# Optimization experiments

Measured on AMD Instinct MI355X. Metric: run time of the kernel, lower is better.

Reference implementation:

```python
import jax, jax.numpy as jnp
import numpy as np

N = 50000   # nodes
E = 800000  # edges
B = 512     # graphs
EPS = 1e-5  # BatchNorm eps


def _p(k, shape, scale=0.05):
    return jax.random.normal(k, shape, dtype=jnp.float32) * scale


def setup_inputs() -> dict:
    key = jax.random.key(0)
    ks = jax.random.split(key, 24)
    inp = {
        "x": jax.random.normal(ks[0], (N, 4), dtype=jnp.float32),
        "edge_index": jax.random.randint(ks[1], (2, E), 0, N, dtype=jnp.int64),
        "edge_weight": jax.random.uniform(ks[2], (E,), dtype=jnp.float32),
        "batch": jnp.sort(jax.random.randint(ks[3], (N,), 0, B, dtype=jnp.int64)),
        # block1: GCNConv(4,64) + BN + shortcut Linear(4,64)
        "W1": _p(ks[4], (4, 64)), "b1": jnp.zeros((64,), jnp.float32),
        "g1": jnp.ones((64,), jnp.float32), "be1": jnp.zeros((64,), jnp.float32),
        "sW1": _p(ks[5], (4, 64)), "sb1": jnp.zeros((64,), jnp.float32),
        # block2: GCNConv(64,64) + BN, identity shortcut
        "W2": _p(ks[6], (64, 64)), "b2": jnp.zeros((64,), jnp.float32),
        "g2": jnp.ones((64,), jnp.float32), "be2": jnp.zeros((64,), jnp.float32),
        # block3: GCNConv(64,128) + BN + shortcut Linear(64,128)
        "W3": _p(ks[7], (64, 128)), "b3": jnp.zeros((128,), jnp.float32),
        "g3": jnp.ones((128,), jnp.float32), "be3": jnp.zeros((128,), jnp.float32),
        "sW3": _p(ks[8], (64, 128)), "sb3": jnp.zeros((128,), jnp.float32),
        # head: Linear(256,128) + BN + ReLU + Linear(128,1)
        "fW1": _p(ks[9], (256, 128)), "fb1": jnp.zeros((128,), jnp.float32),
        "fg": jnp.ones((128,), jnp.float32), "fbe": jnp.zeros((128,), jnp.float32),
        "fW2": _p(ks[10], (128, 1)), "fb2": jnp.zeros((1,), jnp.float32),
    }
    return inp


def _bn(x, g, b):
    # training-mode BatchNorm1d over node dim (biased variance)
    m = x.mean(0)
    v = x.var(0)
    return (x - m) * jax.lax.rsqrt(v + EPS) * g + b


def _gcn(x, W, b, src, dst, w, n):
    # PyG GCNConv: add self-loops (weight 1), symmetric normalization
    h = x @ W  # [n, out]
    loop = jnp.arange(n)
    s = jnp.concatenate([src, loop])
    d = jnp.concatenate([dst, loop])
    ww = jnp.concatenate([w, jnp.ones((n,), x.dtype)])
    deg = jax.ops.segment_sum(ww, d, num_segments=n)
    dis = jnp.where(deg > 0, jax.lax.rsqrt(jnp.maximum(deg, EPS)), 0.0)
    norm = dis[s] * ww * dis[d]  # [E+n]
    return jax.ops.segment_sum(h[s] * norm[:, None], d, num_segments=n) + b


def _block(x, W, b, g, be, sW, sb, src, dst, w, n):
    out = jax.nn.relu(_bn(_gcn(x, W, b, src, dst, w, n), g, be))
    sc = x if sW is None else x @ sW + sb
    return out + sc


def reference(x, edge_index, edge_weight, batch,
              W1, b1, g1, be1, sW1, sb1,
              W2, b2, g2, be2,
              W3, b3, g3, be3, sW3, sb3,
              fW1, fb1, fg, fbe, fW2, fb2):
    n = x.shape[0]
    src, dst = edge_index[0], edge_index[1]
    h = _block(x, W1, b1, g1, be1, sW1, sb1, src, dst, edge_weight, n)
    h = _block(h, W2, b2, g2, be2, None, None, src, dst, edge_weight, n)
    h = _block(h, W3, b3, g3, be3, sW3, sb3, src, dst, edge_weight, n)
    # global mean / max pooling per graph
    cnt = jax.ops.segment_sum(jnp.ones((n,), h.dtype), batch, num_segments=B)
    p1 = jax.ops.segment_sum(h, batch, num_segments=B) / jnp.maximum(cnt, 1.0)[:, None]
    p2 = jax.ops.segment_max(h, batch, num_segments=B)
    z = jnp.concatenate([p1, p2], axis=1)  # [B, 256]
    z = jax.nn.relu(_bn(z @ fW1 + fb1, fg, fbe))  # Dropout eval = identity
    return z @ fW2 + fb2  # [B, 1]
```

## Files before the change

### kernel.cpp

```cpp
#include <hip/hip_runtime.h>

#define BNEPS 1e-5f


__global__ void k_fill(float* p, int n, float v){
  int i = blockIdx.x*blockDim.x + threadIdx.x;
  if(i < n) p[i] = v;
}


__global__ void k_count(int* cnt, const int* __restrict__ dst, int E){
  int e = blockIdx.x*blockDim.x + threadIdx.x;
  if(e < E) atomicAdd(&cnt[dst[e]], 1);
}

__global__ void k_scan1(int* cnt, int* rowptr, int* bsum, int n){
  __shared__ int sh[256];
  int tid = threadIdx.x;
  int i = blockIdx.x*256 + tid;
  int v = (i < n) ? cnt[i] : 0;
  sh[tid] = v;
  __syncthreads();
  for(int o = 1; o < 256; o <<= 1){
    int t = (tid >= o) ? sh[tid-o] : 0;
    __syncthreads();
    sh[tid] += t;
    __syncthreads();
  }
  if(i < n){ rowptr[i] = sh[tid] - v; cnt[i] = 0; }
  if(tid == 255) bsum[blockIdx.x] = sh[255];
}

__global__ void k_scan2(int* bsum, int m){
  __shared__ int sh[256];
  int tid = threadIdx.x;
  int v = (tid < m) ? bsum[tid] : 0;
  sh[tid] = v;
  __syncthreads();
  for(int o = 1; o < 256; o <<= 1){
    int t = (tid >= o) ? sh[tid-o] : 0;
    __syncthreads();
    sh[tid] += t;
    __syncthreads();
  }
  if(tid < m) bsum[tid] = sh[tid] - v;
}

__global__ void k_scan3(int* rowptr, const int* bsum, int n, int E){
  int i = blockIdx.x*blockDim.x + threadIdx.x;
  if(i < n) rowptr[i] += bsum[i >> 8];
  if(i == 0) rowptr[n] = E;
}

__global__ void k_scatter2(const int* __restrict__ src, const int* __restrict__ dst,
                           const float* __restrict__ w, const int* __restrict__ rowptr,
                           int* cur, int2* __restrict__ erec, int E){
  int e = blockIdx.x*blockDim.x + threadIdx.x;
  if(e >= E) return;
  int d = dst[e];
  int idx = rowptr[d] + atomicAdd(&cur[d], 1);
  erec[idx] = make_int2(src[e], __float_as_int(w[e]));
}

__global__ void k_degdis(const int2* __restrict__ erec, const int* __restrict__ rowptr,
                         float* __restrict__ dis, int n){
  int i = blockIdx.x*blockDim.x + threadIdx.x;
  if(i >= n) return;
  float s = 1.0f;
  int e0 = rowptr[i], e1 = rowptr[i+1];
  for(int j = e0; j < e1; j++) s += __int_as_float(erec[j].y);
  dis[i] = rsqrtf(s);
}

__global__ void k_mknorm(int2* __restrict__ erec, const int* __restrict__ rowptr,
                         const float* __restrict__ dis, int n){
  int i = blockIdx.x*blockDim.x + threadIdx.x;
  if(i >= n) return;
  float di = dis[i];
  int e0 = rowptr[i], e1 = rowptr[i+1];
  for(int j = e0; j < e1; j++){
    int2 r = erec[j];
    erec[j].y = __float_as_int(dis[r.x] * __int_as_float(r.y) * di);
  }
}


__global__ __launch_bounds__(256)
void k_gcn1_fused(const float* __restrict__ X, const float* __restrict__ dis,
                  const int* __restrict__ rowptr, const int2* __restrict__ erec,
                  const float* __restrict__ W, const float* __restrict__ bias,
                  float* __restrict__ H, float* __restrict__ stats, int n){
  const int tid = threadIdx.x;
  const int lane = tid & 63;
  const int wid = tid >> 6;
  const int eg = lane >> 2;
  const int ch = lane & 3;
  const float w0 = W[lane], w1 = W[64+lane], w2 = W[128+lane], w3 = W[192+lane];
  const float bc = bias[lane];
  float s = 0.f, s2 = 0.f;
  for(int i = blockIdx.x*4 + wid; i < n; i += gridDim.x*4){
    int e0 = rowptr[i], e1 = rowptr[i+1];
    float acc = 0.f;
    for(int j = e0 + eg; j < e1; j += 16){
      int2 r = erec[j];
      acc += X[(size_t)r.x*4 + ch] * __int_as_float(r.y);
    }
    if(eg == 0){
      float d = dis[i];
      acc += X[(size_t)i*4 + ch] * d * d;
    }
    acc += __shfl_xor(acc, 4);
    acc += __shfl_xor(acc, 8);
    acc += __shfl_xor(acc, 16);
    acc += __shfl_xor(acc, 32);
    float p0 = __shfl(acc, 0), p1 = __shfl(acc, 1);
    float p2 = __shfl(acc, 2), p3 = __shfl(acc, 3);
    float h = bc + p0*w0 + p1*w1 + p2*w2 + p3*w3;
    H[(size_t)i*64 + lane] = h;
    s += h; s2 += h*h;
  }
  __shared__ float rs[256], rs2[256];
  rs[tid] = s; rs2[tid] = s2;
  __syncthreads();
  if(tid < 64){
    atomicAdd(&stats[tid],    rs[tid]+rs[tid+64]+rs[tid+128]+rs[tid+192]);
    atomicAdd(&stats[64+tid], rs2[tid]+rs2[tid+64]+rs2[tid+128]+rs2[tid+192]);
  }
}


template<int C>
__global__ void k_gather(const float* __restrict__ H, const float* __restrict__ dis,
                         const int* __restrict__ rowptr, const int2* __restrict__ erec,
                         float* __restrict__ P, int n){
  const int NPB = 256 / C;
  int i = blockIdx.x*NPB + threadIdx.x / C;
  int c = threadIdx.x % C;
  if(i >= n) return;
  float di = dis[i];
  float acc = H[(size_t)i*C + c]*di*di;
  int e0 = rowptr[i], e1 = rowptr[i+1];
  int j = e0;
  for(; j + 8 <= e1; j += 8){
    int2 r0 = erec[j],   r1 = erec[j+1], r2 = erec[j+2], r3 = erec[j+3];
    int2 r4 = erec[j+4], r5 = erec[j+5], r6 = erec[j+6], r7 = erec[j+7];
    float h0 = H[(size_t)r0.x*C + c];
    float h1 = H[(size_t)r1.x*C + c];
    float h2 = H[(size_t)r2.x*C + c];
    float h3 = H[(size_t)r3.x*C + c];
    float h4 = H[(size_t)r4.x*C + c];
    float h5 = H[(size_t)r5.x*C + c];
    float h6 = H[(size_t)r6.x*C + c];
    float h7 = H[(size_t)r7.x*C + c];
    acc += h0*__int_as_float(r0.y) + h1*__int_as_float(r1.y)
         + h2*__int_as_float(r2.y) + h3*__int_as_float(r3.y)
         + h4*__int_as_float(r4.y) + h5*__int_as_float(r5.y)
         + h6*__int_as_float(r6.y) + h7*__int_as_float(r7.y);
  }
  for(; j < e1; j++){
    int2 r = erec[j];
    acc += H[(size_t)r.x*C + c] * __int_as_float(r.y);
  }
  P[(size_t)i*C + c] = acc;
}


template<int C>
__global__ __launch_bounds__(256)
void k_gemm_tile(const float* __restrict__ X, const float* __restrict__ W,
                 const float* __restrict__ bias, float* __restrict__ H,
                 float* __restrict__ stats, int n, int ntiles){
  const int RR = C/16;
  const int CG = C/4;
  __shared__ float Xs[64*65];
  __shared__ float Ws[64*C];
  __shared__ float sst[2*C];
  const int tid = threadIdx.x;
  const int cg = tid % CG, rg = tid / CG;
  const int c0 = cg*4;
  for(int t = tid; t < 16*C; t += 256)
    reinterpret_cast<float4*>(Ws)[t] = reinterpret_cast<const float4*>(W)[t];
  const float4 bc = *reinterpret_cast<const float4*>(bias + c0);
  float sacc[4] = {0,0,0,0}, qacc[4] = {0,0,0,0};
  const float4* X4 = reinterpret_cast<const float4*>(X);
  for(int tile = blockIdx.x; tile < ntiles; tile += gridDim.x){
    const int r0 = tile*64;
    __syncthreads();
    #pragma unroll
    for(int q = 0; q < 4; q++){
      int idx = tid + q*256;
      int row = idx >> 4, k4 = idx & 15;
      float4 v = (r0+row < n) ? X4[(size_t)(r0+row)*16 + k4] : make_float4(0.f,0.f,0.f,0.f);
      Xs[(4*k4+0)*65 + row] = v.x;
      Xs[(4*k4+1)*65 + row] = v.y;
      Xs[(4*k4+2)*65 + row] = v.z;
      Xs[(4*k4+3)*65 + row] = v.w;
    }
    __syncthreads();
    float acc[RR][4];
    #pragma unroll
    for(int r = 0; r < RR; r++){ acc[r][0]=bc.x; acc[r][1]=bc.y; acc[r][2]=bc.z; acc[r][3]=bc.w; }
    #pragma unroll 8
    for(int k = 0; k < 64; k++){
      float4 wv = reinterpret_cast<const float4*>(Ws)[k*CG + cg];
      #pragma unroll
      for(int r = 0; r < RR; r++){
        float xv = Xs[k*65 + rg*RR + r];
        acc[r][0] = fmaf(xv, wv.x, acc[r][0]);
        acc[r][1] = fmaf(xv, wv.y, acc[r][1]);
        acc[r][2] = fmaf(xv, wv.z, acc[r][2]);
        acc[r][3] = fmaf(xv, wv.w, acc[r][3]);
      }
    }
    #pragma unroll
    for(int r = 0; r < RR; r++){
      int row = r0 + rg*RR + r;
      if(row < n){
        *reinterpret_cast<float4*>(H + (size_t)row*C + c0) =
            make_float4(acc[r][0], acc[r][1], acc[r][2], acc[r][3]);
        #pragma unroll
        for(int j = 0; j < 4; j++){ sacc[j] += acc[r][j]; qacc[j] += acc[r][j]*acc[r][j]; }
      }
    }
  }
  for(int t = tid; t < 2*C; t += 256) sst[t] = 0.f;
  __syncthreads();
  #pragma unroll
  for(int j = 0; j < 4; j++){
    atomicAdd(&sst[c0+j], sacc[j]);
    atomicAdd(&sst[C+c0+j], qacc[j]);
  }
  __syncthreads();
  for(int t = tid; t < 2*C; t += 256) atomicAdd(&stats[t], sst[t]);
}

template<int C>
__global__ __launch_bounds__(256)
void k_gemm_bnsc_tile(const float* __restrict__ X, const float* __restrict__ sW,
                      const float* __restrict__ sb,
                      const float* __restrict__ agg, const float* __restrict__ stats,
                      const float* __restrict__ g, const float* __restrict__ be,
                      float* __restrict__ out, int n, int ntiles){
  const int RR = C/16;
  const int CG = C/4;
  __shared__ float Xs[64*65];
  __shared__ float Ws[64*C];
  const int tid = threadIdx.x;
  const int cg = tid % CG, rg = tid / CG;
  const int c0 = cg*4;
  for(int t = tid; t < 16*C; t += 256)
    reinterpret_cast<float4*>(Ws)[t] = reinterpret_cast<const float4*>(sW)[t];
  const float4 bc = *reinterpret_cast<const float4*>(sb + c0);
  float scal[4], shft[4];
  {
    float invn = 1.0f / n;
    #pragma unroll
    for(int j = 0; j < 4; j++){
      float m = stats[c0+j]*invn;
      float v = stats[C+c0+j]*invn - m*m;
      float rs = rsqrtf(v + BNEPS) * g[c0+j];
      scal[j] = rs;
      shft[j] = be[c0+j] - m*rs;
    }
  }
  const float4* X4 = reinterpret_cast<const float4*>(X);
  for(int tile = blockIdx.x; tile < ntiles; tile += gridDim.x){
    const int r0 = tile*64;
    __syncthreads();
    #pragma unroll
    for(int q = 0; q < 4; q++){
      int idx = tid + q*256;
      int row = idx >> 4, k4 = idx & 15;
      float4 v = (r0+row < n) ? X4[(size_t)(r0+row)*16 + k4] : make_float4(0.f,0.f,0.f,0.f);
      Xs[(4*k4+0)*65 + row] = v.x;
      Xs[(4*k4+1)*65 + row] = v.y;
      Xs[(4*k4+2)*65 + row] = v.z;
      Xs[(4*k4+3)*65 + row] = v.w;
    }
    __syncthreads();
    float acc[RR][4];
    #pragma unroll
    for(int r = 0; r < RR; r++){ acc[r][0]=bc.x; acc[r][1]=bc.y; acc[r][2]=bc.z; acc[r][3]=bc.w; }
    #pragma unroll 8
    for(int k = 0; k < 64; k++){
      float4 wv = reinterpret_cast<const float4*>(Ws)[k*CG + cg];
      #pragma unroll
      for(int r = 0; r < RR; r++){
        float xv = Xs[k*65 + rg*RR + r];
        acc[r][0] = fmaf(xv, wv.x, acc[r][0]);
        acc[r][1] = fmaf(xv, wv.y, acc[r][1]);
        acc[r][2] = fmaf(xv, wv.z, acc[r][2]);
        acc[r][3] = fmaf(xv, wv.w, acc[r][3]);
      }
    }
    #pragma unroll
    for(int r = 0; r < RR; r++){
      int row = r0 + rg*RR + r;
      if(row < n){
        float4 a = *reinterpret_cast<const float4*>(agg + (size_t)row*C + c0);
        float4 o;
        o.x = fmaxf(a.x*scal[0] + shft[0], 0.f) + acc[r][0];
        o.y = fmaxf(a.y*scal[1] + shft[1], 0.f) + acc[r][1];
        o.z = fmaxf(a.z*scal[2] + shft[2], 0.f) + acc[r][2];
        o.w = fmaxf(a.w*scal[3] + shft[3], 0.f) + acc[r][3];
        *reinterpret_cast<float4*>(out + (size_t)row*C + c0) = o;
      }
    }
  }
}


template<int C>
__global__ void k_bn_add4(const float* __restrict__ agg, const float* __restrict__ stats,
                          const float* __restrict__ g, const float* __restrict__ be,
                          const float* __restrict__ add, float* __restrict__ out, int n){
  int idx = blockIdx.x*blockDim.x + threadIdx.x;
  if(idx >= n*(C/4)) return;
  int c = (idx % (C/4))*4;
  float invn = 1.0f / n;
  float4 sm = *reinterpret_cast<const float4*>(stats + c);
  float4 sq = *reinterpret_cast<const float4*>(stats + C + c);
  float4 g4 = *reinterpret_cast<const float4*>(g + c);
  float4 b4 = *reinterpret_cast<const float4*>(be + c);
  float4 a  = reinterpret_cast<const float4*>(agg)[idx];
  float4 ad = reinterpret_cast<const float4*>(add)[idx];
  float4 o;
  #define BN1(X) { float m = sm.X*invn; float v = sq.X*invn - m*m; \
    o.X = fmaxf((a.X-m)*rsqrtf(v+BNEPS)*g4.X + b4.X, 0.f) + ad.X; }
  BN1(x) BN1(y) BN1(z) BN1(w)
  #undef BN1
  reinterpret_cast<float4*>(out)[idx] = o;
}

__global__ void k_bn_sc4_v4(const float* __restrict__ agg, const float* __restrict__ stats,
                            const float* __restrict__ g, const float* __restrict__ be,
                            const float* __restrict__ X, const float* __restrict__ sW,
                            const float* __restrict__ sb, float* __restrict__ out, int n){
  int idx = blockIdx.x*blockDim.x + threadIdx.x;
  if(idx >= n*16) return;
  int i = idx >> 4;
  int c = (idx & 15)*4;
  float invn = 1.0f / n;
  float4 xr = *reinterpret_cast<const float4*>(X + (size_t)i*4);
  float4 s0 = *reinterpret_cast<const float4*>(sW + c);
  float4 s1 = *reinterpret_cast<const float4*>(sW + 64 + c);
  float4 s2 = *reinterpret_cast<const float4*>(sW + 128 + c);
  float4 s3 = *reinterpret_cast<const float4*>(sW + 192 + c);
  float4 sb4 = *reinterpret_cast<const float4*>(sb + c);
  float4 sm = *reinterpret_cast<const float4*>(stats + c);
  float4 sq = *reinterpret_cast<const float4*>(stats + 64 + c);
  float4 g4 = *reinterpret_cast<const float4*>(g + c);
  float4 b4 = *reinterpret_cast<const float4*>(be + c);
  float4 a  = reinterpret_cast<const float4*>(agg)[idx];
  float4 o;
  #define BN1(X) { float sc = xr.x*s0.X + xr.y*s1.X + xr.z*s2.X + xr.w*s3.X + sb4.X; \
    float m = sm.X*invn; float v = sq.X*invn - m*m; \
    o.X = fmaxf((a.X-m)*rsqrtf(v+BNEPS)*g4.X + b4.X, 0.f) + sc; }
  BN1(x) BN1(y) BN1(z) BN1(w)
  #undef BN1
  reinterpret_cast<float4*>(out)[idx] = o;
}


__global__ void k_pool(const float* __restrict__ H, const int* __restrict__ batch,
                       float* __restrict__ z, int n){
  int b = blockIdx.x, c = threadIdx.x;
  int lo = 0, hi = n;
  while(lo < hi){ int mid = (lo+hi)>>1; if(batch[mid] <  b) lo = mid+1; else hi = mid; }
  int start = lo;
  hi = n;
  while(lo < hi){ int mid = (lo+hi)>>1; if(batch[mid] <  b+1) lo = mid+1; else hi = mid; }
  int end = lo;
  float s = 0.f, mx = -INFINITY;
  for(int i = start; i < end; i++){
    float v = H[(size_t)i*128 + c];
    s += v; mx = fmaxf(mx, v);
  }
  int cnt = end - start;
  z[b*256 + c]       = s / fmaxf((float)cnt, 1.f);
  z[b*256 + 128 + c] = mx;
}

__global__ void k_head1(const float* __restrict__ z, const float* __restrict__ fW1,
                        const float* __restrict__ fb1, float* __restrict__ zr,
                        float* __restrict__ stats, int B){
  int idx = blockIdx.x*blockDim.x + threadIdx.x;
  int tid = threadIdx.x;
  float acc = 0.f;
  if(idx < B*128){
    int b = idx >> 7, c = idx & 127;
    acc = fb1[c];
    #pragma unroll 4
    for(int k = 0; k < 256; k++) acc = fmaf(z[b*256+k], fW1[k*128+c], acc);
    zr[idx] = acc;
  }
  __shared__ float rs[256], rs2[256];
  rs[tid] = acc; rs2[tid] = acc*acc;
  __syncthreads();
  if(tid < 128){
    atomicAdd(&stats[tid],     rs[tid]+rs[tid+128]);
    atomicAdd(&stats[128+tid], rs2[tid]+rs2[tid+128]);
  }
}

__global__ void k_final(const float* __restrict__ zr, const float* __restrict__ stats,
                        const float* __restrict__ fg, const float* __restrict__ fbe,
                        const float* __restrict__ fW2, const float* __restrict__ fb2,
                        float* __restrict__ out, int B){
  __shared__ float red[128];
  int b = blockIdx.x, c = threadIdx.x;
  float invn = 1.0f / B;
  float m  = stats[c]*invn;
  float v  = stats[128+c]*invn - m*m;
  float rs = rsqrtf(v + BNEPS);
  float val = fmaxf((zr[b*128+c]-m)*rs*fg[c] + fbe[c], 0.f) * fW2[c];
  red[c] = val;
  __syncthreads();
  for(int s = 64; s > 0; s >>= 1){
    if(c < s) red[c] += red[c+s];
    __syncthreads();
  }
  if(c == 0) out[b] = red[0] + fb2[0];
}


extern "C" void kernel_launch(void* const* d_in, const int* in_sizes, int n_in,
                              void* d_out, int out_size, void* d_ws, size_t ws_size,
                              hipStream_t stream){
  const float* x   = (const float*)d_in[0];
  const int*   ei  = (const int*)  d_in[1];
  const float* ew  = (const float*)d_in[2];
  const int*   bat = (const int*)  d_in[3];
  const float* W1  = (const float*)d_in[4];  const float* b1  = (const float*)d_in[5];
  const float* g1  = (const float*)d_in[6];  const float* be1 = (const float*)d_in[7];
  const float* sW1 = (const float*)d_in[8];  const float* sb1 = (const float*)d_in[9];
  const float* W2  = (const float*)d_in[10]; const float* b2  = (const float*)d_in[11];
  const float* g2  = (const float*)d_in[12]; const float* be2 = (const float*)d_in[13];
  const float* W3  = (const float*)d_in[14]; const float* b3  = (const float*)d_in[15];
  const float* g3  = (const float*)d_in[16]; const float* be3 = (const float*)d_in[17];
  const float* sW3 = (const float*)d_in[18]; const float* sb3 = (const float*)d_in[19];
  const float* fW1 = (const float*)d_in[20]; const float* fb1 = (const float*)d_in[21];
  const float* fg  = (const float*)d_in[22]; const float* fbe = (const float*)d_in[23];
  const float* fW2 = (const float*)d_in[24]; const float* fb2 = (const float*)d_in[25];
  float* out = (float*)d_out;

  const int n = in_sizes[0] / 4;
  const int E = in_sizes[2];
  const int B = out_size;
  const int* src = ei;
  const int* dst = ei + E;

  auto GB = [](long long t){ return (int)((t + 255) / 256); };
  const int nscanb = (n + 255) / 256;
  const int ntiles = (n + 63) / 64;

  float* ws = (float*)d_ws;
  size_t off = 0;
  auto alloc = [&](size_t cnt)->float*{ float* p = ws + off; off += (cnt + 63) & ~size_t(63); return p; };

  const size_t npad = ((size_t)n + 63) & ~size_t(63);
  float* bufA  = alloc((size_t)n * 64);
  float* hbuf  = alloc((size_t)n * 128);
  float* agg   = alloc((size_t)n * 128);
  float* z     = alloc((size_t)B * 256);
  float* zr    = alloc((size_t)B * 128);
  float* zreg  = alloc(npad + 1024);
  int*   cnt   = (int*)zreg;
  float* st1 = zreg + npad; float* st2 = st1 + 256;
  float* st3 = st2 + 256;   float* stH = st3 + 256;
  float* dis    = alloc(n);
  int*   rowptr = (int*)alloc(n + 1);
  int*   bsum   = (int*)alloc(256);
  int2*  erec   = (int2*)alloc((size_t)E * 2);

  k_fill<<<GB(npad + 1024),256,0,stream>>>(zreg, (int)(npad + 1024), 0.f);
  k_count<<<GB(E),256,0,stream>>>(cnt, dst, E);
  k_scan1<<<nscanb,256,0,stream>>>(cnt, rowptr, bsum, n);
  k_scan2<<<1,256,0,stream>>>(bsum, nscanb);
  k_scan3<<<GB(n),256,0,stream>>>(rowptr, bsum, n, E);
  k_scatter2<<<GB(E),256,0,stream>>>(src, dst, ew, rowptr, cnt, erec, E);
  k_degdis<<<GB(n),256,0,stream>>>(erec, rowptr, dis, n);
  k_mknorm<<<GB(n),256,0,stream>>>(erec, rowptr, dis, n);

  float* P = hbuf;
  k_gcn1_fused<<<512,256,0,stream>>>(x, dis, rowptr, erec, W1, b1, agg, st1, n);
  k_bn_sc4_v4<<<GB((long long)n*16),256,0,stream>>>(agg, st1, g1, be1, x, sW1, sb1, bufA, n);

  k_gather<64><<<(n+3)/4,256,0,stream>>>(bufA, dis, rowptr, erec, P, n);
  k_gemm_tile<64><<<512,256,0,stream>>>(P, W2, b2, agg, st2, n, ntiles);
  k_bn_add4<64><<<GB((long long)n*16),256,0,stream>>>(agg, st2, g2, be2, bufA, bufA, n);

  k_gather<64><<<(n+3)/4,256,0,stream>>>(bufA, dis, rowptr, erec, P, n);
  k_gemm_tile<128><<<512,256,0,stream>>>(P, W3, b3, agg, st3, n, ntiles);
  k_gemm_bnsc_tile<128><<<512,256,0,stream>>>(bufA, sW3, sb3, agg, st3, g3, be3, hbuf, n, ntiles);

  k_pool<<<B,128,0,stream>>>(hbuf, bat, z, n);
  k_head1<<<GB((long long)B*128),256,0,stream>>>(z, fW1, fb1, zr, stH, B);
  k_final<<<B,128,0,stream>>>(zr, stH, fg, fbe, fW2, fb2, out, B);
}
```

Before: 487.5 us.

## Build CSR via two-level bucketed scatter with fused degree computation

Replaces the single random scatter of edges into CSR with two passes. The first scatters edges into coarse bins of 128 destination nodes, packing the local node id with the source index. The second reorders each bin into CSR order, where writes stay local, and computes the degree rsqrt in the same kernel, removing the separate degree kernel. This aims to improve memory locality of the scatter and reduce atomic contention spread over the whole array. The cost is an extra edge buffer, one more full read and write of the edge records, and a fallback path that depends on node count and workspace size.

```diff
diff --git a/kernel.cpp b/kernel.cpp
--- a/kernel.cpp
+++ b/kernel.cpp
@@ -50,6 +50,41 @@
   int i = blockIdx.x*blockDim.x + threadIdx.x;
   if(i < n) rowptr[i] += bsum[i >> 8];
   if(i == 0) rowptr[n] = E;
+}
+
+__global__ void k_binscat(const int* __restrict__ src, const int* __restrict__ dst,
+                          const float* __restrict__ w, const int* __restrict__ rowptr,
+                          int* bincur, int2* __restrict__ binbuf, int E){
+  int e = blockIdx.x*blockDim.x + threadIdx.x;
+  if(e >= E) return;
+  int d = dst[e];
+  int bin = d >> 7;
+  int base = rowptr[bin << 7];
+  int idx = base + atomicAdd(&bincur[bin], 1);
+  binbuf[idx] = make_int2(((d & 127) << 17) | src[e], __float_as_int(w[e]));
+}
+
+__global__ void k_binsort(const int2* __restrict__ binbuf, const int* __restrict__ rowptr,
+                          int* cur, int2* __restrict__ erec, float* __restrict__ dis, int n){
+  int bin = blockIdx.x;
+  int node0 = bin << 7;
+  int node1 = min(node0 + 128, n);
+  int e0 = rowptr[node0];
+  int e1 = rowptr[node1];
+  for(int j = e0 + threadIdx.x; j < e1; j += blockDim.x){
+    int2 r = binbuf[j];
+    int d = node0 + ((unsigned)r.x >> 17);
+    int s = r.x & 0x1FFFF;
+    int idx = rowptr[d] + atomicAdd(&cur[d], 1);
+    erec[idx] = make_int2(s, r.y);
+  }
+  __syncthreads();
+  for(int i = node0 + threadIdx.x; i < node1; i += blockDim.x){
+    float sm = 1.0f;
+    int a = rowptr[i], b = rowptr[i+1];
+    for(int j = a; j < b; j++) sm += __int_as_float(erec[j].y);
+    dis[i] = rsqrtf(sm);
+  }
 }
 
 __global__ void k_scatter2(const int* __restrict__ src, const int* __restrict__ dst,
@@ -453,6 +488,7 @@
   auto GB = [](long long t){ return (int)((t + 255) / 256); };
   const int nscanb = (n + 255) / 256;
   const int ntiles = (n + 63) / 64;
+  const int nbins  = (n + 127) >> 7;
 
   float* ws = (float*)d_ws;
   size_t off = 0;
@@ -464,22 +500,33 @@
   float* agg   = alloc((size_t)n * 128);
   float* z     = alloc((size_t)B * 256);
   float* zr    = alloc((size_t)B * 128);
-  float* zreg  = alloc(npad + 1024);
+  float* zreg  = alloc(npad + 512 + 1024);
   int*   cnt   = (int*)zreg;
-  float* st1 = zreg + npad; float* st2 = st1 + 256;
-  float* st3 = st2 + 256;   float* stH = st3 + 256;
+  int*   bincur= (int*)(zreg + npad);
+  float* st1 = zreg + npad + 512; float* st2 = st1 + 256;
+  float* st3 = st2 + 256;         float* stH = st3 + 256;
   float* dis    = alloc(n);
   int*   rowptr = (int*)alloc(n + 1);
   int*   bsum   = (int*)alloc(256);
   int2*  erec   = (int2*)alloc((size_t)E * 2);
-
-  k_fill<<<GB(npad + 1024),256,0,stream>>>(zreg, (int)(npad + 1024), 0.f);
+  size_t off_nobin = off;
+  int2*  binbuf = (int2*)alloc((size_t)E * 2);
+
+  const bool use_bins = (n <= (1 << 17)) && (nbins <= 512) &&
+                        (ws_size >= off * sizeof(float));
+
+  k_fill<<<GB(npad + 512 + 1024),256,0,stream>>>(zreg, (int)(npad + 512 + 1024), 0.f);
   k_count<<<GB(E),256,0,stream>>>(cnt, dst, E);
   k_scan1<<<nscanb,256,0,stream>>>(cnt, rowptr, bsum, n);
   k_scan2<<<1,256,0,stream>>>(bsum, nscanb);
   k_scan3<<<GB(n),256,0,stream>>>(rowptr, bsum, n, E);
-  k_scatter2<<<GB(E),256,0,stream>>>(src, dst, ew, rowptr, cnt, erec, E);
-  k_degdis<<<GB(n),256,0,stream>>>(erec, rowptr, dis, n);
+  if(use_bins){
+    k_binscat<<<GB(E),256,0,stream>>>(src, dst, ew, rowptr, bincur, binbuf, E);
+    k_binsort<<<nbins,256,0,stream>>>(binbuf, rowptr, cnt, erec, dis, n);
+  } else {
+    k_scatter2<<<GB(E),256,0,stream>>>(src, dst, ew, rowptr, cnt, erec, E);
+    k_degdis<<<GB(n),256,0,stream>>>(erec, rowptr, dis, n);
+  }
   k_mknorm<<<GB(n),256,0,stream>>>(erec, rowptr, dis, n);
 
   float* P = hbuf;
```

After: 744.4 us. +52.7%, slower.

## Replace scatter-pass atomics with 8-way sharded counts and stored edge ranks

Applied to the files above, without the earlier changes.

The CSR build now counts edges into 8 sharded histograms, picked by block index, and records each edge's rank from the counting atomic. The scan then computes per-shard offsets, so the scatter pass writes each edge to its slot without a second atomic. This removes one full pass of atomics and spreads contention on hot destination nodes across shards. The cost is 8x larger count and offset arrays to zero and scan, plus an extra rank array of size E to write and read.

```diff
diff --git a/kernel.cpp b/kernel.cpp
--- a/kernel.cpp
+++ b/kernel.cpp
@@ -9,16 +9,26 @@
 }
 
 
-__global__ void k_count(int* cnt, const int* __restrict__ dst, int E){
+__global__ void k_count8(int* cnt8, int* rank, const int* __restrict__ dst, int E, int npad){
   int e = blockIdx.x*blockDim.x + threadIdx.x;
-  if(e < E) atomicAdd(&cnt[dst[e]], 1);
-}
-
-__global__ void k_scan1(int* cnt, int* rowptr, int* bsum, int n){
+  if(e < E){
+    int s = blockIdx.x & 7;
+    rank[e] = atomicAdd(&cnt8[s*npad + dst[e]], 1);
+  }
+}
+
+__global__ void k_scan1(const int* __restrict__ cnt8, int* __restrict__ sbase,
+                        int* rowptr, int* bsum, int n, int npad){
   __shared__ int sh[256];
   int tid = threadIdx.x;
   int i = blockIdx.x*256 + tid;
-  int v = (i < n) ? cnt[i] : 0;
+  int v = 0;
+  if(i < n){
+    int run = 0;
+    #pragma unroll
+    for(int s = 0; s < 8; s++){ sbase[s*npad + i] = run; run += cnt8[s*npad + i]; }
+    v = run;
+  }
   sh[tid] = v;
   __syncthreads();
   for(int o = 1; o < 256; o <<= 1){
@@ -27,7 +37,7 @@
     sh[tid] += t;
     __syncthreads();
   }
-  if(i < n){ rowptr[i] = sh[tid] - v; cnt[i] = 0; }
+  if(i < n) rowptr[i] = sh[tid] - v;
   if(tid == 255) bsum[blockIdx.x] = sh[255];
 }
 
@@ -54,12 +64,13 @@
 
 __global__ void k_scatter2(const int* __restrict__ src, const int* __restrict__ dst,
                            const float* __restrict__ w, const int* __restrict__ rowptr,
-                           int* cur, int2* __restrict__ erec, int E){
+                           const int* __restrict__ sbase, const int* __restrict__ rank,
+                           int2* __restrict__ erec, int E, int npad){
   int e = blockIdx.x*blockDim.x + threadIdx.x;
   if(e >= E) return;
   int d = dst[e];
-  int idx = rowptr[d] + atomicAdd(&cur[d], 1);
-  erec[idx] = make_int2(src[e], __float_as_int(w[e]));
+  int s = blockIdx.x & 7;
+  erec[rowptr[d] + sbase[s*npad + d] + rank[e]] = make_int2(src[e], __float_as_int(w[e]));
 }
 
 __global__ void k_degdis(const int2* __restrict__ erec, const int* __restrict__ rowptr,
@@ -464,21 +475,23 @@
   float* agg   = alloc((size_t)n * 128);
   float* z     = alloc((size_t)B * 256);
   float* zr    = alloc((size_t)B * 128);
-  float* zreg  = alloc(npad + 1024);
-  int*   cnt   = (int*)zreg;
-  float* st1 = zreg + npad; float* st2 = st1 + 256;
-  float* st3 = st2 + 256;   float* stH = st3 + 256;
+  float* zreg  = alloc(8*npad + 1024);
+  int*   cnt8  = (int*)zreg;
+  float* st1 = zreg + 8*npad; float* st2 = st1 + 256;
+  float* st3 = st2 + 256;     float* stH = st3 + 256;
+  int*   sbase  = (int*)alloc(8*npad);
   float* dis    = alloc(n);
   int*   rowptr = (int*)alloc(n + 1);
   int*   bsum   = (int*)alloc(256);
+  int*   rank   = (int*)alloc(E);
   int2*  erec   = (int2*)alloc((size_t)E * 2);
 
-  k_fill<<<GB(npad + 1024),256,0,stream>>>(zreg, (int)(npad + 1024), 0.f);
-  k_count<<<GB(E),256,0,stream>>>(cnt, dst, E);
-  k_scan1<<<nscanb,256,0,stream>>>(cnt, rowptr, bsum, n);
+  k_fill<<<GB(8*npad + 1024),256,0,stream>>>(zreg, (int)(8*npad + 1024), 0.f);
+  k_count8<<<GB(E),256,0,stream>>>(cnt8, rank, dst, E, (int)npad);
+  k_scan1<<<nscanb,256,0,stream>>>(cnt8, sbase, rowptr, bsum, n, (int)npad);
   k_scan2<<<1,256,0,stream>>>(bsum, nscanb);
   k_scan3<<<GB(n),256,0,stream>>>(rowptr, bsum, n, E);
-  k_scatter2<<<GB(E),256,0,stream>>>(src, dst, ew, rowptr, cnt, erec, E);
+  k_scatter2<<<GB(E),256,0,stream>>>(src, dst, ew, rowptr, sbase, rank, erec, E, (int)npad);
   k_degdis<<<GB(n),256,0,stream>>>(erec, rowptr, dis, n);
   k_mknorm<<<GB(n),256,0,stream>>>(erec, rowptr, dis, n);
 
```

Result: faster. 454.0 us (-6.9%).
